# Kernel tuning notes

Measured on AMD Instinct MI355X. Metric: run time of the kernel, lower is better.

## Reference

```python
import jax, jax.numpy as jnp
import numpy as np

N, E, F_DIM = 30000, 480000, 256
CLS_HID, NUM_CLASS, GEN_HID, MI_HID, BATCH = 128, 16, 64, 128, 4096
COM_L1, COM_L2, LAM, ALPHA, TAU, EPS = 0.5, 0.5, 0.5, 1.0, 0.5, 1e-8


def _glorot(key, shape):
    scale = jnp.sqrt(2.0 / (shape[0] + shape[-1]))
    return scale * jax.random.normal(key, shape, dtype=jnp.float32)


def setup_inputs() -> dict:
    key = jax.random.key(0)
    ks = jax.random.split(key, 32)
    inp = {
        'feat': jax.random.normal(ks[0], (N, F_DIM), dtype=jnp.float32),
        'view1_indices': jax.random.randint(ks[1], (2, E), 0, N),
        'view1_values': jax.random.uniform(ks[2], (E,), dtype=jnp.float32),
        'view2_indices': jax.random.randint(ks[3], (2, E), 0, N),
        'view2_values': jax.random.uniform(ks[4], (E,), dtype=jnp.float32),
        'idx': jnp.sort(jax.random.randint(ks[5], (BATCH,), 0, N)),
        # GenView (v1 and v2): gen_gcn weight + gen_mlp (Linear(2*gen_hid, 1))
        'W_gen_v1': _glorot(ks[6], (F_DIM, GEN_HID)),
        'Wm_v1': _glorot(ks[7], (2 * GEN_HID, 1)),
        'bm_v1': jnp.zeros((1,), dtype=jnp.float32),
        'W_gen_v2': _glorot(ks[8], (F_DIM, GEN_HID)),
        'Wm_v2': _glorot(ks[9], (2 * GEN_HID, 1)),
        'bm_v2': jnp.zeros((1,), dtype=jnp.float32),
        # Classification: three two-layer GCN encoders (v1, v2, v)
        'W1_v1': _glorot(ks[10], (F_DIM, CLS_HID)), 'W2_v1': _glorot(ks[11], (CLS_HID, NUM_CLASS)),
        'W1_v2': _glorot(ks[12], (F_DIM, CLS_HID)), 'W2_v2': _glorot(ks[13], (CLS_HID, NUM_CLASS)),
        'W1_v': _glorot(ks[14], (F_DIM, CLS_HID)), 'W2_v': _glorot(ks[15], (CLS_HID, NUM_CLASS)),
        # MI_NCE: three single GCN layers + shared projection MLP
        'Wg': _glorot(ks[16], (F_DIM, MI_HID)),
        'Wg1': _glorot(ks[17], (F_DIM, MI_HID)),
        'Wg2': _glorot(ks[18], (F_DIM, MI_HID)),
        'Wp1': _glorot(ks[19], (MI_HID, MI_HID)), 'bp1': jnp.zeros((MI_HID,), dtype=jnp.float32),
        'Wp2': _glorot(ks[20], (MI_HID, MI_HID)), 'bp2': jnp.zeros((MI_HID,), dtype=jnp.float32),
    }
    return inp


def spmm(idx, vals, x, n):
    # sparse COO adj (idx [2,E], vals [E]) @ dense x [n,d]
    return jax.ops.segment_sum(vals[:, None] * x[idx[1]], idx[0], num_segments=n)


def gcn_layer(x, idx, vals, W, n, act):
    h = spmm(idx, vals, x @ W, n)
    return jax.nn.relu(h) if act else h


def two_layer(x, idx, vals, W1, W2, n):
    return gcn_layer(gcn_layer(x, idx, vals, W1, n, True), idx, vals, W2, n, False)


def sparse_row_softmax(scores, rows, n):
    m = jax.lax.stop_gradient(jax.ops.segment_max(scores, rows, num_segments=n))
    e = jnp.exp(scores - m[rows])
    s = jax.ops.segment_sum(e, rows, num_segments=n)
    return e / s[rows]


def gen_view(feat, idx, vals, Wg, Wm, bm, com_lambda, n):
    emb = gcn_layer(feat, idx, vals, Wg, n, True)
    ff = jnp.concatenate([emb[idx[0]], emb[idx[1]]], axis=-1)  # [E, 2*gen_hid]
    temp = (ff @ Wm + bm).reshape(-1)
    pi = sparse_row_softmax(temp, idx[0], n)  # torch.sparse.softmax(dim=1)
    return vals + com_lambda * pi  # same sparsity pattern as v_ori


def sym(idx, vals):
    # normalize1 (big=True): adj + adj.T as COO concat (duplicates sum in spmm)
    return jnp.concatenate([idx, idx[::-1]], axis=1), jnp.concatenate([vals, vals])


def get_weight(prob):
    top2 = jax.lax.top_k(prob, 2)[0]
    fir, sec = top2[:, 0], top2[:, 1]
    return jnp.exp(ALPHA * (LAM * jnp.log(fir + EPS) + (1.0 - LAM) * jnp.log(fir - sec + EPS)))


def contrast_cal(z1, z2):
    num = z1 @ z2.T
    den = jnp.linalg.norm(z1, axis=-1, keepdims=True) @ jnp.linalg.norm(z2, axis=-1, keepdims=True).T
    m12 = jnp.exp(num / den / TAU)
    m21 = m12.T
    l12 = -jnp.log(jnp.diag(m12 / (m12.sum(1, keepdims=True) + EPS)) + EPS).mean()
    l21 = -jnp.log(jnp.diag(m21 / (m21.sum(1, keepdims=True) + EPS)) + EPS).mean()
    return 0.5 * (l12 + l21)


def cogsl_forward(feat, view1_values, view2_values,
                  W_gen_v1, Wm_v1, bm_v1, W_gen_v2, Wm_v2, bm_v2,
                  W1_v1, W2_v1, W1_v2, W2_v2, W1_v, W2_v,
                  Wg, Wg1, Wg2, Wp1, bp1, Wp2, bp2,
                  view1_indices, view2_indices, idx):
    n = feat.shape[0]
    # View_Estimator (GenView + normalize1)
    nv1 = gen_view(feat, view1_indices, view1_values, W_gen_v1, Wm_v1, bm_v1, COM_L1, n)
    nv2 = gen_view(feat, view2_indices, view2_values, W_gen_v2, Wm_v2, bm_v2, COM_L2, n)
    i1, v1 = sym(view1_indices, nv1)
    i2, v2 = sym(view2_indices, nv2)
    # Classification on each generated view
    prob_v1 = jax.nn.softmax(two_layer(feat, i1, v1, W1_v1, W2_v1, n), axis=1)
    prob_v2 = jax.nn.softmax(two_layer(feat, i2, v2, W1_v2, W2_v2, n), axis=1)
    logits_v1 = jnp.log(prob_v1 + EPS)
    logits_v2 = jnp.log(prob_v2 + EPS)
    # Fusion: per-node convex combination of the two sparse views (row scaling)
    w1 = get_weight(prob_v1)
    w2 = get_weight(prob_v2)
    b1 = w1 / (w1 + w2)
    b2 = w2 / (w1 + w2)
    idx_f = jnp.concatenate([i1, i2], axis=1)
    vals_f = jnp.concatenate([b1[i1[0]] * v1, b2[i2[0]] * v2])
    prob_v = jax.nn.softmax(two_layer(feat, idx_f, vals_f, W1_v, W2_v, n), axis=1)
    logits_v = jnp.log(prob_v + EPS)
    # MI_NCE over [fused v, v1, v2], big=True -> sample `batch` nodes
    proj = lambda h: jax.nn.elu(h @ Wp1 + bp1) @ Wp2 + bp2
    ev = proj(gcn_layer(feat, idx_f, vals_f, Wg, n, True))[idx]
    e1 = proj(gcn_layer(feat, i1, v1, Wg1, n, True))[idx]
    e2 = proj(gcn_layer(feat, i2, v2, Wg2, n, True))[idx]
    vv1 = contrast_cal(ev, e1)
    vv2 = contrast_cal(ev, e2)
    v1v2 = contrast_cal(e1, e2)
    return jnp.concatenate([logits_v.ravel(), logits_v1.ravel(), logits_v2.ravel(),
                            jnp.stack([vv1, vv2, v1v2])])


def reference(feat, view1_indices, view1_values, view2_indices, view2_values, idx,
              W_gen_v1, Wm_v1, bm_v1, W_gen_v2, Wm_v2, bm_v2,
              W1_v1, W2_v1, W1_v2, W2_v2, W1_v, W2_v,
              Wg, Wg1, Wg2, Wp1, bp1, Wp2, bp2):
    return cogsl_forward(feat, view1_values, view2_values,
                         W_gen_v1, Wm_v1, bm_v1, W_gen_v2, Wm_v2, bm_v2,
                         W1_v1, W2_v1, W1_v2, W2_v2, W1_v, W2_v,
                         Wg, Wg1, Wg2, Wp1, bp1, Wp2, bp2,
                         view1_indices, view2_indices, idx)
```

## Files before the change

kernel.cpp:

```cpp
#include <hip/hip_runtime.h>
#include <math.h>

#define NN 30000
#define EE 480000
#define FD 256
#define CH 128
#define NCLS 16
#define GH 64
#define MH 128
#define BT 4096
#define EPSc 1e-8f
#define GBc ((NN + 127) / 128)
#define SPB8 ((NN + 7) / 8)
#define SPB16 ((NN + 15) / 16)
#define RBc ((BT + 15) / 16)

typedef __attribute__((ext_vector_type(8))) short short8;
typedef __attribute__((ext_vector_type(4))) float f32x4;

__device__ __forceinline__ unsigned short f2bf(float x) {
    unsigned b = __float_as_uint(x);
    unsigned r = b + 0x7FFFu + ((b >> 16) & 1u);
    return (unsigned short)(r >> 16);
}
__device__ __forceinline__ float bf2f(unsigned short h) {
    return __uint_as_float(((unsigned)h) << 16);
}
__device__ __forceinline__ float4 fma4(float s, float4 x, float4 a) {
    a.x = fmaf(s, x.x, a.x); a.y = fmaf(s, x.y, a.y);
    a.z = fmaf(s, x.z, a.z); a.w = fmaf(s, x.w, a.w);
    return a;
}

__global__ void split_bf16(const float* __restrict__ x, unsigned short* __restrict__ hi,
                           unsigned short* __restrict__ lo, long n) {
    long i = (long)blockIdx.x * 256 + threadIdx.x;
    if (i >= n) return;
    float v = x[i];
    unsigned short h = f2bf(v);
    hi[i] = h;
    lo[i] = f2bf(v - bf2f(h));
}

struct WSArgs {
    const float* s[8];
    unsigned short* h[8];
    unsigned short* l[8];
};
__global__ void wsplit_all(WSArgs a) {
    constexpr int NNp[8] = {64, 64, 128, 128, 128, 128, 128, 128};
    constexpr int OFF[9] = {0, 16384, 32768, 65536, 98304, 131072, 163840, 196608, 229376};
    int i = blockIdx.x * 256 + threadIdx.x;
    if (i >= 229376) return;
    int w = 0;
#pragma unroll
    for (int t = 1; t < 8; t++) if (i >= OFF[t]) w = t;
    int j = i - OFF[w];
    int N = NNp[w];
    int k = j / N, n = j % N;
    float v = a.s[w][j];
    unsigned short hh = f2bf(v);
    a.h[w][(size_t)n * 256 + k] = hh;
    a.l[w][(size_t)n * 256 + k] = f2bf(v - bf2f(hh));
}

template <int NT, bool OUT16>
__device__ __forceinline__ void gemm3_body(
    unsigned short* sm, int bx,
    const unsigned short* __restrict__ Ahi, const unsigned short* __restrict__ Alo,
    const unsigned short* __restrict__ BThi, const unsigned short* __restrict__ BTlo,
    int K, void* __restrict__ Cv, int Cstride, int M)
{
    unsigned short* Ah = sm;
    unsigned short* Al = Ah + 128 * 40;
    unsigned short* Bh = Al + 128 * 40;
    unsigned short* Bl = Bh + NT * 16 * 40;
    int t = threadIdx.x;
    int w = t >> 6, l = t & 63;
    int lane = l & 15, quad = l >> 4;
    int row0 = bx * 128;
    f32x4 acc[2][NT];
#pragma unroll
    for (int s = 0; s < 2; s++)
#pragma unroll
        for (int n = 0; n < NT; n++) acc[s][n] = (f32x4)(0.f);

    int ar = t >> 1, ako = (t & 1) << 4;
    int nkc = K >> 5;
    for (int kc = 0; kc < nkc; kc++) {
        int kb = kc << 5;
        {
            int gr = row0 + ar;
            float4 h0, h1, l0, l1;
            if (gr < M) {
                const float4* pH = (const float4*)&Ahi[(size_t)gr * K + kb + ako];
                const float4* pL = (const float4*)&Alo[(size_t)gr * K + kb + ako];
                h0 = pH[0]; h1 = pH[1]; l0 = pL[0]; l1 = pL[1];
            } else {
                h0 = h1 = l0 = l1 = make_float4(0.f, 0.f, 0.f, 0.f);
            }
            float4* dH = (float4*)&Ah[ar * 40 + ako];
            dH[0] = h0; dH[1] = h1;
            float4* dL = (float4*)&Al[ar * 40 + ako];
            dL[0] = l0; dL[1] = l1;
        }
        if (ar < NT * 16) {
            const float4* pH = (const float4*)&BThi[(size_t)ar * K + kb + ako];
            const float4* pL = (const float4*)&BTlo[(size_t)ar * K + kb + ako];
            float4 h0 = pH[0], h1 = pH[1], l0 = pL[0], l1 = pL[1];
            float4* dH = (float4*)&Bh[ar * 40 + ako];
            dH[0] = h0; dH[1] = h1;
            float4* dL = (float4*)&Bl[ar * 40 + ako];
            dL[0] = l0; dL[1] = l1;
        }
        __syncthreads();
        short8 aH[2], aL[2];
#pragma unroll
        for (int s = 0; s < 2; s++) {
            int r = w * 32 + s * 16 + lane;
            aH[s] = *(const short8*)&Ah[r * 40 + quad * 8];
            aL[s] = *(const short8*)&Al[r * 40 + quad * 8];
        }
#pragma unroll
        for (int n = 0; n < NT; n++) {
            int r = n * 16 + lane;
            short8 bH = *(const short8*)&Bh[r * 40 + quad * 8];
            short8 bL = *(const short8*)&Bl[r * 40 + quad * 8];
#pragma unroll
            for (int s = 0; s < 2; s++) {
                acc[s][n] = __builtin_amdgcn_mfma_f32_16x16x32_bf16(aH[s], bH, acc[s][n], 0, 0, 0);
                acc[s][n] = __builtin_amdgcn_mfma_f32_16x16x32_bf16(aH[s], bL, acc[s][n], 0, 0, 0);
                acc[s][n] = __builtin_amdgcn_mfma_f32_16x16x32_bf16(aL[s], bH, acc[s][n], 0, 0, 0);
            }
        }
        __syncthreads();
    }
#pragma unroll
    for (int s = 0; s < 2; s++) {
        int rb = row0 + w * 32 + s * 16 + quad * 4;
#pragma unroll
        for (int reg = 0; reg < 4; reg++) {
            int gr = rb + reg;
            if (gr >= M) continue;
#pragma unroll
            for (int n = 0; n < NT; n++) {
                if (OUT16)
                    ((unsigned short*)Cv)[(size_t)gr * Cstride + n * 16 + lane] = f2bf(acc[s][n][reg]);
                else
                    ((float*)Cv)[(size_t)gr * Cstride + n * 16 + lane] = acc[s][n][reg];
            }
        }
    }
}

template <int NT, bool OUT16>
__device__ __forceinline__ void gemm1_body(
    unsigned short* sm, int bx,
    const unsigned short* __restrict__ Ahi,
    const unsigned short* __restrict__ BThi,
    int K, void* __restrict__ Cv, int Cstride, int M)
{
    unsigned short* Ah = sm;
    unsigned short* Bh = Ah + 128 * 40;
    int t = threadIdx.x;
    int w = t >> 6, l = t & 63;
    int lane = l & 15, quad = l >> 4;
    int row0 = bx * 128;
    f32x4 acc[2][NT];
#pragma unroll
    for (int s = 0; s < 2; s++)
#pragma unroll
        for (int n = 0; n < NT; n++) acc[s][n] = (f32x4)(0.f);

    int ar = t >> 1, ako = (t & 1) << 4;
    int nkc = K >> 5;
    for (int kc = 0; kc < nkc; kc++) {
        int kb = kc << 5;
        {
            int gr = row0 + ar;
            float4 h0, h1;
            if (gr < M) {
                const float4* pH = (const float4*)&Ahi[(size_t)gr * K + kb + ako];
                h0 = pH[0]; h1 = pH[1];
            } else {
                h0 = h1 = make_float4(0.f, 0.f, 0.f, 0.f);
            }
            float4* dH = (float4*)&Ah[ar * 40 + ako];
            dH[0] = h0; dH[1] = h1;
        }
        if (ar < NT * 16) {
            const float4* pH = (const float4*)&BThi[(size_t)ar * K + kb + ako];
            float4 h0 = pH[0], h1 = pH[1];
            float4* dH = (float4*)&Bh[ar * 40 + ako];
            dH[0] = h0; dH[1] = h1;
        }
        __syncthreads();
        short8 aH[2];
#pragma unroll
        for (int s = 0; s < 2; s++)
            aH[s] = *(const short8*)&Ah[(w * 32 + s * 16 + lane) * 40 + quad * 8];
#pragma unroll
        for (int n = 0; n < NT; n++) {
            short8 bH = *(const short8*)&Bh[(n * 16 + lane) * 40 + quad * 8];
#pragma unroll
            for (int s = 0; s < 2; s++)
                acc[s][n] = __builtin_amdgcn_mfma_f32_16x16x32_bf16(aH[s], bH, acc[s][n], 0, 0, 0);
        }
        __syncthreads();
    }
#pragma unroll
    for (int s = 0; s < 2; s++) {
        int rb = row0 + w * 32 + s * 16 + quad * 4;
#pragma unroll
        for (int reg = 0; reg < 4; reg++) {
            int gr = rb + reg;
            if (gr >= M) continue;
#pragma unroll
            for (int n = 0; n < NT; n++) {
                if (OUT16)
                    ((unsigned short*)Cv)[(size_t)gr * Cstride + n * 16 + lane] = f2bf(acc[s][n][reg]);
                else
                    ((float*)Cv)[(size_t)gr * Cstride + n * 16 + lane] = acc[s][n][reg];
            }
        }
    }
}

__global__ __launch_bounds__(256) void mega0(
    const int* __restrict__ i1, const int* __restrict__ i2, int* __restrict__ cnt,
    int* __restrict__ sd1, int* __restrict__ sd2,
    int* __restrict__ sc1, int* __restrict__ sc2,
    const unsigned short* __restrict__ feat_hi,
    const unsigned short* __restrict__ w1vh, unsigned short* __restrict__ Ph2,
    const unsigned short* __restrict__ wgallh, unsigned short* __restrict__ Pmi16)
{
    __shared__ unsigned short sm[128 * 40 + 8 * 16 * 40];
    int b = blockIdx.x;
    if (b < GBc) {
        gemm1_body<8, true>(sm, b, feat_hi, w1vh, FD, Ph2, 128, NN);
        return;
    }
    b -= GBc;
    if (b < 3 * GBc) {
        int y = b / GBc, bx = b % GBc;
        gemm1_body<8, true>(sm, bx, feat_hi, wgallh + (size_t)y * 32768,
                            FD, Pmi16 + (size_t)y * 128, 384, NN);
        return;
    }
    b -= 3 * GBc;
    int e = b * 256 + threadIdx.x;
    if (e >= EE) return;
    int r1 = i1[e], c1 = i1[EE + e];
    int r2 = i2[e], c2 = i2[EE + e];
    sd1[e] = atomicAdd(&cnt[r1], 1);
    sd2[e] = atomicAdd(&cnt[NN + r2], 1);
    sc1[e] = atomicAdd(&cnt[2 * NN + c1], 1);
    sc2[e] = atomicAdd(&cnt[3 * NN + c2], 1);
}

__global__ __launch_bounds__(256) void mega1(
    const int* __restrict__ i1, const float* __restrict__ v1,
    const int* __restrict__ i2, const float* __restrict__ v2,
    const int* __restrict__ sd1, const int* __restrict__ sd2,
    const int* __restrict__ sc1, const int* __restrict__ sc2,
    const int* __restrict__ rp4,
    int2* __restrict__ ed1, int2* __restrict__ ec1,
    int2* __restrict__ ed2, int2* __restrict__ ec2,
    const unsigned short* __restrict__ feat_hi, const unsigned short* __restrict__ feat_lo,
    const unsigned short* __restrict__ wgen12h, const unsigned short* __restrict__ wgen12l,
    float* __restrict__ Pg,
    const unsigned short* __restrict__ w1pairh, const unsigned short* __restrict__ w1pairl,
    float* __restrict__ P01)
{
    __shared__ unsigned short sm[128 * 40 * 2 + 8 * 16 * 40 * 2];
    int b = blockIdx.x;
    if (b < GBc) {
        gemm3_body<8, false>(sm, b, feat_hi, feat_lo, wgen12h, wgen12l, FD, Pg, 128, NN);
        return;
    }
    b -= GBc;
    if (b < 2 * GBc) {
        int y = b / GBc, bx = b % GBc;
        gemm3_body<8, false>(sm, bx, feat_hi, feat_lo,
                             w1pairh + (size_t)y * 32768, w1pairl + (size_t)y * 32768,
                             FD, P01 + (size_t)y * 128, 256, NN);
        return;
    }
    b -= 2 * GBc;
    int e = b * 256 + threadIdx.x;
    if (e >= EE) return;
    const int* rp_d1 = rp4;
    const int* rp_d2 = rp4 + (NN + 1);
    const int* rp_c1 = rp4 + 2 * (NN + 1);
    const int* rp_c2 = rp4 + 3 * (NN + 1);
    int r = i1[e], c = i1[EE + e];
    int p = rp_d1[r] + sd1[e];
    ed1[p] = make_int2(c, __float_as_int(v1[e]));
    ec1[rp_c1[c] + sc1[e]] = make_int2(r, p);
    r = i2[e]; c = i2[EE + e];
    p = rp_d2[r] + sd2[e];
    ed2[p] = make_int2(c, __float_as_int(v2[e]));
    ec2[rp_c2[c] + sc2[e]] = make_int2(r, p);
}

__global__ __launch_bounds__(256) void contrast_direct(
    const unsigned short* __restrict__ z16, float* __restrict__ stats)
{
    int p = blockIdx.z;
    int pa = (p == 2) ? 1 : 0;
    int pb = (p == 0) ? 1 : 2;
    const unsigned short* A = z16 + (size_t)pa * BT * MH;
    const unsigned short* B = z16 + (size_t)pb * BT * MH;
    float* diag = stats + (size_t)p * 3 * BT;
    float* rs = diag + BT;
    float* cs = rs + BT;
    int t = threadIdx.x;
    int w = t >> 6, l = t & 63, m = l & 15, quad = l >> 4;
    int i0 = blockIdx.y * 128, j0 = blockIdx.x * 128;
// ... 127 lines not shown
template <int STR4>
__device__ __forceinline__ void gath_dir_f32(
    const int* __restrict__ rp, const int2* __restrict__ ed, int row,
    const float4* __restrict__ x4, int xo, float4* a)
{
    int p0 = rp[row], p1 = rp[row + 1];
    int j = p0;
    for (; j + 8 <= p1; j += 8) {
        int2 q0 = ed[j], q1 = ed[j+1], q2 = ed[j+2], q3 = ed[j+3];
        int2 q4 = ed[j+4], q5 = ed[j+5], q6 = ed[j+6], q7 = ed[j+7];
        float4 x0 = x4[(size_t)q0.x * STR4 + xo];
        float4 x1 = x4[(size_t)q1.x * STR4 + xo];
        float4 x2 = x4[(size_t)q2.x * STR4 + xo];
        float4 x3 = x4[(size_t)q3.x * STR4 + xo];
        float4 x5 = x4[(size_t)q4.x * STR4 + xo];
        float4 x6 = x4[(size_t)q5.x * STR4 + xo];
        float4 x7 = x4[(size_t)q6.x * STR4 + xo];
        float4 x8 = x4[(size_t)q7.x * STR4 + xo];
        a[0] = fma4(__int_as_float(q0.y), x0, a[0]);
        a[1] = fma4(__int_as_float(q1.y), x1, a[1]);
        a[2] = fma4(__int_as_float(q2.y), x2, a[2]);
        a[3] = fma4(__int_as_float(q3.y), x3, a[3]);
        a[0] = fma4(__int_as_float(q4.y), x5, a[0]);
        a[1] = fma4(__int_as_float(q5.y), x6, a[1]);
        a[2] = fma4(__int_as_float(q6.y), x7, a[2]);
        a[3] = fma4(__int_as_float(q7.y), x8, a[3]);
    }
    for (; j + 4 <= p1; j += 4) {
        int2 q0 = ed[j], q1 = ed[j+1], q2 = ed[j+2], q3 = ed[j+3];
        a[0] = fma4(__int_as_float(q0.y), x4[(size_t)q0.x * STR4 + xo], a[0]);
        a[1] = fma4(__int_as_float(q1.y), x4[(size_t)q1.x * STR4 + xo], a[1]);
        a[2] = fma4(__int_as_float(q2.y), x4[(size_t)q2.x * STR4 + xo], a[2]);
        a[3] = fma4(__int_as_float(q3.y), x4[(size_t)q3.x * STR4 + xo], a[3]);
    }
    for (; j < p1; j++) {
        int2 q = ed[j];
        a[0] = fma4(__int_as_float(q.y), x4[(size_t)q.x * STR4 + xo], a[0]);
    }
}
template <int STR4>
__device__ __forceinline__ void gath_csc_f32(
    const int* __restrict__ rp, const int2* __restrict__ ec, const float* __restrict__ nvd,
    int row, const float4* __restrict__ x4, int xo, float4* a)
{
    int p0 = rp[row], p1 = rp[row + 1];
    int j = p0;
    for (; j + 8 <= p1; j += 8) {
        int2 q0 = ec[j], q1 = ec[j+1], q2 = ec[j+2], q3 = ec[j+3];
        int2 q4 = ec[j+4], q5 = ec[j+5], q6 = ec[j+6], q7 = ec[j+7];
        float4 x0 = x4[(size_t)q0.x * STR4 + xo];
        float4 x1 = x4[(size_t)q1.x * STR4 + xo];
        float4 x2 = x4[(size_t)q2.x * STR4 + xo];
        float4 x3 = x4[(size_t)q3.x * STR4 + xo];
        float4 x5 = x4[(size_t)q4.x * STR4 + xo];
        float4 x6 = x4[(size_t)q5.x * STR4 + xo];
        float4 x7 = x4[(size_t)q6.x * STR4 + xo];
        float4 x8 = x4[(size_t)q7.x * STR4 + xo];
        float v0 = nvd[q0.y], v1 = nvd[q1.y], v2 = nvd[q2.y], v3 = nvd[q3.y];
        float v4 = nvd[q4.y], v5 = nvd[q5.y], v6 = nvd[q6.y], v7 = nvd[q7.y];
        a[0] = fma4(v0, x0, a[0]);
        a[1] = fma4(v1, x1, a[1]);
        a[2] = fma4(v2, x2, a[2]);
        a[3] = fma4(v3, x3, a[3]);
        a[0] = fma4(v4, x5, a[0]);
        a[1] = fma4(v5, x6, a[1]);
        a[2] = fma4(v6, x7, a[2]);
        a[3] = fma4(v7, x8, a[3]);
    }
    for (; j + 4 <= p1; j += 4) {
        int2 q0 = ec[j], q1 = ec[j+1], q2 = ec[j+2], q3 = ec[j+3];
        float v0 = nvd[q0.y], v1 = nvd[q1.y], v2 = nvd[q2.y], v3 = nvd[q3.y];
        a[0] = fma4(v0, x4[(size_t)q0.x * STR4 + xo], a[0]);
        a[1] = fma4(v1, x4[(size_t)q1.x * STR4 + xo], a[1]);
        a[2] = fma4(v2, x4[(size_t)q2.x * STR4 + xo], a[2]);
        a[3] = fma4(v3, x4[(size_t)q3.x * STR4 + xo], a[3]);
    }
    for (; j < p1; j++) {
        int2 q = ec[j];
        a[0] = fma4(nvd[q.y], x4[(size_t)q.x * STR4 + xo], a[0]);
    }
}

__global__ __launch_bounds__(256) void spmm64_scores(
    const int* __restrict__ rp_d, const int2* __restrict__ e1, const int2* __restrict__ e2,
    const float* __restrict__ Pg, const float* __restrict__ Wm1,
    const float* __restrict__ Wm2, float* __restrict__ sb)
{
    int y = blockIdx.y;
    const int* rp = rp_d + y * (NN + 1);
    const int2* arr = y ? e2 : e1;
    int row = blockIdx.x * 16 + threadIdx.x / 16;
    int o = threadIdx.x % 16;
    if (row >= NN) return;
    float4 a[4] = {};
    gath_dir_f32<32>(rp, arr, row, (const float4*)Pg, y * 16 + o, a);
    float4 r;
    r.x = fmaxf((a[0].x + a[1].x) + (a[2].x + a[3].x), 0.f);
    r.y = fmaxf((a[0].y + a[1].y) + (a[2].y + a[3].y), 0.f);
    r.z = fmaxf((a[0].z + a[1].z) + (a[2].z + a[3].z), 0.f);
    r.w = fmaxf((a[0].w + a[1].w) + (a[2].w + a[3].w), 0.f);
    const float* Wmh = (y ? Wm2 : Wm1) + GH;
    float part = r.x * Wmh[o * 4] + r.y * Wmh[o * 4 + 1]
               + r.z * Wmh[o * 4 + 2] + r.w * Wmh[o * 4 + 3];
    part += __shfl_xor(part, 1); part += __shfl_xor(part, 2);
    part += __shfl_xor(part, 4); part += __shfl_xor(part, 8);
    if (o == 0) sb[y * NN + row] = part;
}

__device__ __forceinline__ void softmax16_epi(
    float4 r, int node, float* __restrict__ logits, float* __restrict__ wout)
{
    int o = threadIdx.x & 3;
    float mx = fmaxf(fmaxf(r.x, r.y), fmaxf(r.z, r.w));
    mx = fmaxf(mx, __shfl_xor(mx, 1));
    mx = fmaxf(mx, __shfl_xor(mx, 2));
    float e0 = expf(r.x - mx), e1 = expf(r.y - mx), e2 = expf(r.z - mx), e3 = expf(r.w - mx);
    float s = (e0 + e1) + (e2 + e3);
    s += __shfl_xor(s, 1);
    s += __shfl_xor(s, 2);
    float inv = 1.f / s;
    float p0 = e0 * inv, p1 = e1 * inv, p2 = e2 * inv, p3 = e3 * inv;
    float4 lg;
    lg.x = logf(p0 + EPSc); lg.y = logf(p1 + EPSc);
    lg.z = logf(p2 + EPSc); lg.w = logf(p3 + EPSc);
    ((float4*)logits)[(size_t)node * 4 + o] = lg;
    if (wout) {
        float f = p0, se = -1.f;
        if (p1 > f) { se = f; f = p1; } else se = p1;
        if (p2 > f) { se = f; f = p2; } else if (p2 > se) se = p2;
        if (p3 > f) { se = f; f = p3; } else if (p3 > se) se = p3;
#pragma unroll
        for (int d = 1; d <= 2; d <<= 1) {
            float of = __shfl_xor(f, d), os = __shfl_xor(se, d);
            if (of > f) { se = fmaxf(f, os); f = of; }
            else se = fmaxf(se, of);
        }
        if (o == 0)
            wout[node] = expf(0.5f * logf(f + EPSc) + 0.5f * logf(f - se + EPSc));
    }
}

__global__ __launch_bounds__(256) void spmm16_softmax_pair(
    const int* __restrict__ rp_d, const int* __restrict__ rp_c,
    const int2* __restrict__ ed1, const int2* __restrict__ ec1, const float* __restrict__ nvd1,
    const int2* __restrict__ ed2, const int2* __restrict__ ec2, const float* __restrict__ nvd2,
    const float* __restrict__ R01, float* __restrict__ logits_base, float* __restrict__ w12)
{
    int y = blockIdx.y;
    const int* rpd = rp_d + y * (NN + 1);
    const int* rpc = rp_c + y * (NN + 1);
    const int2* ed = y ? ed2 : ed1;
    const int2* ec = y ? ec2 : ec1;
    const float* nvd = y ? nvd2 : nvd1;
    int row = blockIdx.x * 64 + threadIdx.x / 4;
    int o = threadIdx.x % 4;
    if (row >= NN) return;
    const float4* x4 = (const float4*)(R01 + (size_t)y * NN * 16);
    float4 a[4] = {};
    gath_dir_f32<4>(rpd, ed, row, x4, o, a);
    gath_csc_f32<4>(rpc, ec, nvd, row, x4, o, a);
    float4 r;
    r.x = (a[0].x + a[1].x) + (a[2].x + a[3].x);
    r.y = (a[0].y + a[1].y) + (a[2].y + a[3].y);
    r.z = (a[0].z + a[1].z) + (a[2].z + a[3].z);
    r.w = (a[0].w + a[1].w) + (a[2].w + a[3].w);
    softmax16_epi(r, row, logits_base + (size_t)y * NN * NCLS, w12 + (size_t)y * NN);
}

__global__ __launch_bounds__(256) void spmm16_fused_softmax(
    const int* __restrict__ rp_d, const int* __restrict__ rp_c,
    const int2* __restrict__ ed1, const int2* __restrict__ ec1, const float* __restrict__ nvd1,
    const int2* __restrict__ ed2, const int2* __restrict__ ec2, const float* __restrict__ nvd2,
    const float* __restrict__ w12, const float* __restrict__ x, float* __restrict__ logits)
{
    int row = blockIdx.x * 64 + threadIdx.x / 4;
    int o = threadIdx.x % 4;
    if (row >= NN) return;
    const float4* x4 = (const float4*)x;
    float4 a[4] = {};
    gath_dir_f32<4>(rp_d, ed1, row, x4, o, a);
    gath_csc_f32<4>(rp_c, ec1, nvd1, row, x4, o, a);
    float4 s1;
    s1.x = (a[0].x + a[1].x) + (a[2].x + a[3].x);
    s1.y = (a[0].y + a[1].y) + (a[2].y + a[3].y);
    s1.z = (a[0].z + a[1].z) + (a[2].z + a[3].z);
    s1.w = (a[0].w + a[1].w) + (a[2].w + a[3].w);
    float4 b[4] = {};
    gath_dir_f32<4>(rp_d + (NN + 1), ed2, row, x4, o, b);
    gath_csc_f32<4>(rp_c + (NN + 1), ec2, nvd2, row, x4, o, b);
    float4 s2;
    s2.x = (b[0].x + b[1].x) + (b[2].x + b[3].x);
    s2.y = (b[0].y + b[1].y) + (b[2].y + b[3].y);
    s2.z = (b[0].z + b[1].z) + (b[2].z + b[3].z);
    s2.w = (b[0].w + b[1].w) + (b[2].w + b[3].w);
    float wa = w12[row], wb = w12[NN + row];
    float inv = 1.f / (wa + wb);
    float w1 = wa * inv, w2 = wb * inv;
    float4 r;
    r.x = w1 * s1.x + w2 * s2.x;
    r.y = w1 * s1.y + w2 * s2.y;
    r.z = w1 * s1.z + w2 * s2.z;
    r.w = w1 * s1.w + w2 * s2.w;
    softmax16_epi(r, row, logits, nullptr);
}

__device__ __forceinline__ void gath_dir_b16(
    const int* __restrict__ rp, const int2* __restrict__ ed, int row,
    const unsigned short* __restrict__ X, int xstride, int o, float* acc)
{
    int p0 = rp[row], p1 = rp[row + 1];
    int j = p0;
    for (; j + 8 <= p1; j += 8) {
        int2 q[8]; short8 x[8];
#pragma unroll
        for (int e = 0; e < 8; e++) q[e] = ed[j + e];
#pragma unroll
        for (int e = 0; e < 8; e++)
            x[e] = *(const short8*)&X[(size_t)q[e].x * xstride + o * 8];
#pragma unroll
        for (int e = 0; e < 8; e++) {
            float v = __int_as_float(q[e].y);
#pragma unroll
            for (int k = 0; k < 8; k++)
                acc[k] = fmaf(v, bf2f((unsigned short)x[e][k]), acc[k]);
        }
    }
    for (; j + 4 <= p1; j += 4) {
        int2 q0 = ed[j], q1 = ed[j+1], q2 = ed[j+2], q3 = ed[j+3];
        short8 x0 = *(const short8*)&X[(size_t)q0.x * xstride + o * 8];
        short8 x1 = *(const short8*)&X[(size_t)q1.x * xstride + o * 8];
        short8 x2 = *(const short8*)&X[(size_t)q2.x * xstride + o * 8];
        short8 x3 = *(const short8*)&X[(size_t)q3.x * xstride + o * 8];
        float v0 = __int_as_float(q0.y), v1 = __int_as_float(q1.y);
        float v2 = __int_as_float(q2.y), v3 = __int_as_float(q3.y);
#pragma unroll
        for (int k = 0; k < 8; k++) {
            acc[k] = fmaf(v0, bf2f((unsigned short)x0[k]), acc[k]);
            acc[k] = fmaf(v1, bf2f((unsigned short)x1[k]), acc[k]);
            acc[k] = fmaf(v2, bf2f((unsigned short)x2[k]), acc[k]);
            acc[k] = fmaf(v3, bf2f((unsigned short)x3[k]), acc[k]);
        }
    }
    for (; j < p1; j++) {
        int2 q = ed[j];
        short8 xv = *(const short8*)&X[(size_t)q.x * xstride + o * 8];
        float v = __int_as_float(q.y);
#pragma unroll
        for (int k = 0; k < 8; k++)
            acc[k] = fmaf(v, bf2f((unsigned short)xv[k]), acc[k]);
    }
}
__device__ __forceinline__ void gath_csc_b16(
    const int* __restrict__ rp, const int2* __restrict__ ec, const float* __restrict__ nvd,
    int row, const unsigned short* __restrict__ X, int xstride, int o, float* acc)
{
    int p0 = rp[row], p1 = rp[row + 1];
    int j = p0;
    for (; j + 8 <= p1; j += 8) {
        int2 q[8]; short8 x[8];
#pragma unroll
        for (int e = 0; e < 8; e++) q[e] = ec[j + e];
#pragma unroll
        for (int e = 0; e < 8; e++)
            x[e] = *(const short8*)&X[(size_t)q[e].x * xstride + o * 8];
        float v[8];
#pragma unroll
        for (int e = 0; e < 8; e++) v[e] = nvd[q[e].y];
#pragma unroll
        for (int e = 0; e < 8; e++) {
#pragma unroll
            for (int k = 0; k < 8; k++)
                acc[k] = fmaf(v[e], bf2f((unsigned short)x[e][k]), acc[k]);
        }
    }
    for (; j + 4 <= p1; j += 4) {
        int2 q0 = ec[j], q1 = ec[j+1], q2 = ec[j+2], q3 = ec[j+3];
        short8 x0 = *(const short8*)&X[(size_t)q0.x * xstride + o * 8];
        short8 x1 = *(const short8*)&X[(size_t)q1.x * xstride + o * 8];
        short8 x2 = *(const short8*)&X[(size_t)q2.x * xstride + o * 8];
        short8 x3 = *(const short8*)&X[(size_t)q3.x * xstride + o * 8];
        float v0 = nvd[q0.y], v1 = nvd[q1.y], v2 = nvd[q2.y], v3 = nvd[q3.y];
#pragma unroll
        for (int k = 0; k < 8; k++) {
            acc[k] = fmaf(v0, bf2f((unsigned short)x0[k]), acc[k]);
            acc[k] = fmaf(v1, bf2f((unsigned short)x1[k]), acc[k]);
            acc[k] = fmaf(v2, bf2f((unsigned short)x2[k]), acc[k]);
            acc[k] = fmaf(v3, bf2f((unsigned short)x3[k]), acc[k]);
        }
    }
    for (; j < p1; j++) {
        int2 q = ec[j];
        short8 xv = *(const short8*)&X[(size_t)q.x * xstride + o * 8];
        float v = nvd[q.y];
#pragma unroll
        for (int k = 0; k < 8; k++)
            acc[k] = fmaf(v, bf2f((unsigned short)xv[k]), acc[k]);
    }
}

__device__ __forceinline__ void rows_b16_body(
    int bx, int y, const int* __restrict__ rp_d, const int* __restrict__ rp_c,
    const int2* __restrict__ ed1, const int2* __restrict__ ec1, const float* __restrict__ nvd1,
    const int2* __restrict__ ed2, const int2* __restrict__ ec2, const float* __restrict__ nvd2,
    const float* __restrict__ w12, const int* __restrict__ rows,
    const unsigned short* __restrict__ Pmi, float* __restrict__ zQ)
{
    int ri = bx * 16 + threadIdx.x / 16;
    int o = threadIdx.x % 16;
    if (ri >= BT) return;
    int node = rows[ri];
    int xoff = (y == 0) ? 0 : ((y == 1) ? 128 : 256);
    const unsigned short* X = Pmi + xoff;
    float acc[8] = {};
    if (y == 0) {
        float a1[8] = {}, a2[8] = {};
        gath_dir_b16(rp_d, ed1, node, X, 384, o, a1);
        gath_csc_b16(rp_c, ec1, nvd1, node, X, 384, o, a1);
        gath_dir_b16(rp_d + (NN + 1), ed2, node, X, 384, o, a2);
        gath_csc_b16(rp_c + (NN + 1), ec2, nvd2, node, X, 384, o, a2);
        float wa = w12[node], wb = w12[NN + node];
        float inv = 1.f / (wa + wb);
        float w1 = wa * inv, w2 = wb * inv;
#pragma unroll
        for (int k = 0; k < 8; k++) acc[k] = w1 * a1[k] + w2 * a2[k];
    } else if (y == 1) {
        gath_dir_b16(rp_d, ed1, node, X, 384, o, acc);
        gath_csc_b16(rp_c, ec1, nvd1, node, X, 384, o, acc);
    } else {
        gath_dir_b16(rp_d + (NN + 1), ed2, node, X, 384, o, acc);
        gath_csc_b16(rp_c + (NN + 1), ec2, nvd2, node, X, 384, o, acc);
    }
    float* out = zQ + ((size_t)y * BT + ri) * 128 + o * 8;
#pragma unroll
    for (int k = 0; k < 8; k++) out[k] = fmaxf(acc[k], 0.f);
}

__device__ __forceinline__ void spmm128f_body(
    float* sm, int bx, int y, const int* __restrict__ rp_d, const int* __restrict__ rp_c,
    const int2* __restrict__ ed, const int2* __restrict__ ec, const float* __restrict__ nvd,
    const float* __restrict__ P01, const float* __restrict__ W2, float* __restrict__ R01)
{
    float* W2s = sm;
    float* Qs  = sm + 2048;
    for (int i = threadIdx.x; i < 2048; i += 256) W2s[i] = W2[i];
    int r = threadIdx.x / 32;
    int o = threadIdx.x % 32;
    int row = bx * 8 + r;
    float4 a[4] = {};
    if (row < NN) {
        gath_dir_f32<64>(rp_d + y * (NN + 1), ed, row, (const float4*)P01, y * 32 + o, a);
        gath_csc_f32<64>(rp_c + y * (NN + 1), ec, nvd, row, (const float4*)P01, y * 32 + o, a);
    }
    float4 q;
    q.x = fmaxf((a[0].x + a[1].x) + (a[2].x + a[3].x), 0.f);
    q.y = fmaxf((a[0].y + a[1].y) + (a[2].y + a[3].y), 0.f);
    q.z = fmaxf((a[0].z + a[1].z) + (a[2].z + a[3].z), 0.f);
    q.w = fmaxf((a[0].w + a[1].w) + (a[2].w + a[3].w), 0.f);
    *(float4*)&Qs[r * 128 + o * 4] = q;
    __syncthreads();
    int t = threadIdx.x;
    if (t < 128) {
        int rr = t >> 4, c = t & 15;
        int grow = bx * 8 + rr;
        if (grow < NN) {
            float acc = 0.f;
            const float* qrow = &Qs[rr * 128];
#pragma unroll 8
            for (int k = 0; k < 128; k++)
                acc = fmaf(qrow[k], W2s[k * 16 + c], acc);
            R01[((size_t)y * NN + grow) * 16 + c] = acc;
        }
    }
}

__device__ __forceinline__ void fused128b2_body(
    float* sm, int bx, const int* __restrict__ rp_d, const int* __restrict__ rp_c,
    const int2* __restrict__ ed1, const int2* __restrict__ ec1, const float* __restrict__ nvd1,
    const int2* __restrict__ ed2, const int2* __restrict__ ec2, const float* __restrict__ nvd2,
    const float* __restrict__ w12, const unsigned short* __restrict__ Ph2,
    const float* __restrict__ W2v, float* __restrict__ R2)
{
    float* W2s = sm;
    float* Qs  = sm + 2048;
    for (int i = threadIdx.x; i < 2048; i += 256) W2s[i] = W2v[i];
    int r = threadIdx.x / 16;
    int o = threadIdx.x % 16;
    int row = bx * 16 + r;
    float a1[8] = {}, a2[8] = {};
    float w1 = 0.f, w2 = 0.f;
    if (row < NN) {
        gath_dir_b16(rp_d, ed1, row, Ph2, 128, o, a1);
        gath_csc_b16(rp_c, ec1, nvd1, row, Ph2, 128, o, a1);
        gath_dir_b16(rp_d + (NN + 1), ed2, row, Ph2, 128, o, a2);
        gath_csc_b16(rp_c + (NN + 1), ec2, nvd2, row, Ph2, 128, o, a2);
        float wa = w12[row], wb = w12[NN + row];
        float inv = 1.f / (wa + wb);
        w1 = wa * inv; w2 = wb * inv;
    }
#pragma unroll
    for (int k = 0; k < 8; k++)
        Qs[r * 128 + o * 8 + k] = fmaxf(w1 * a1[k] + w2 * a2[k], 0.f);
    __syncthreads();
    int t = threadIdx.x;
    int rr = t >> 4, c = t & 15;
    int grow = bx * 16 + rr;
    if (grow < NN) {
        float acc = 0.f;
        const float* qrow = &Qs[rr * 128];
#pragma unroll 8
        for (int k = 0; k < 128; k++)
            acc = fmaf(qrow[k], W2s[k * 16 + c], acc);
        R2[(size_t)grow * 16 + c] = acc;
    }
}

__global__ __launch_bounds__(256) void mega2(
    const int* __restrict__ rp_d, const int* __restrict__ rp_c,
    const int2* __restrict__ ed1, const int2* __restrict__ ec1, const float* __restrict__ nvd1,
    const int2* __restrict__ ed2, const int2* __restrict__ ec2, const float* __restrict__ nvd2,
    const float* __restrict__ P01, const float* __restrict__ W2v1, const float* __restrict__ W2v2,
    float* __restrict__ R01,
    const int* __restrict__ rows, const unsigned short* __restrict__ Pmi,
    float* __restrict__ zQ)
{
    __shared__ float sm[2048 + 8 * 128];
    int b = blockIdx.x;
    if (b < 2 * SPB8) {
        int y = b / SPB8;
        spmm128f_body(sm, b % SPB8, y, rp_d, rp_c, y ? ed2 : ed1, y ? ec2 : ec1,
                      y ? nvd2 : nvd1, P01, y ? W2v2 : W2v1, R01);
        return;
    }
    b -= 2 * SPB8;
    int y = 1 + b / RBc;
    rows_b16_body(b % RBc, y, rp_d, rp_c, ed1, ec1, nvd1, ed2, ec2, nvd2,
                  nullptr, rows, Pmi, zQ);
}

__global__ __launch_bounds__(256) void mega3(
    const int* __restrict__ rp_d, const int* __restrict__ rp_c,
    const int2* __restrict__ ed1, const int2* __restrict__ ec1, const float* __restrict__ nvd1,
    const int2* __restrict__ ed2, const int2* __restrict__ ec2, const float* __restrict__ nvd2,
    const float* __restrict__ w12, const unsigned short* __restrict__ Ph2,
    const float* __restrict__ W2v, float* __restrict__ R2,
    const int* __restrict__ rows, const unsigned short* __restrict__ Pmi,
    float* __restrict__ zQ)
{
    __shared__ float sm[2048 + 16 * 128];
    int b = blockIdx.x;
    if (b < SPB16) {
        fused128b2_body(sm, b, rp_d, rp_c, ed1, ec1, nvd1, ed2, ec2, nvd2,
                        w12, Ph2, W2v, R2);
        return;
    }
    rows_b16_body(b - SPB16, 0, rp_d, rp_c, ed1, ec1, nvd1, ed2, ec2, nvd2,
                  w12, rows, Pmi, zQ);
}

__global__ __launch_bounds__(256) void proj_norm8(
    const float* __restrict__ zQ,
    const float* __restrict__ Wp1, const float* __restrict__ bp1,
    const float* __restrict__ Wp2, const float* __restrict__ bp2,
    unsigned short* __restrict__ z16)
{
    __shared__ float g[8 * MH], u[8 * MH];
    __shared__ float red[4][4];
    int t = threadIdx.x;
    size_t base = (size_t)blockIdx.y * BT + (size_t)blockIdx.x * 8;
    for (int idx = t; idx < 8 * MH; idx += 256)
        g[idx] = zQ[(base + (idx >> 7)) * MH + (idx & 127)];
    __syncthreads();
    int col = t & 127;
    int rh = t >> 7;
    float acc[4];
    float b1 = bp1[col];
#pragma unroll
    for (int rr = 0; rr < 4; rr++) acc[rr] = b1;
    for (int k = 0; k < MH; k++) {
        float wk = Wp1[k * MH + col];
#pragma unroll
        for (int rr = 0; rr < 4; rr++)
            acc[rr] = fmaf(g[(rh * 4 + rr) * MH + k], wk, acc[rr]);
    }
#pragma unroll
    for (int rr = 0; rr < 4; rr++)
        u[(rh * 4 + rr) * MH + col] = acc[rr] > 0.f ? acc[rr] : (expf(acc[rr]) - 1.f);
    __syncthreads();
    float z[4];
    float b2 = bp2[col];
#pragma unroll
    for (int rr = 0; rr < 4; rr++) z[rr] = b2;
    for (int k = 0; k < MH; k++) {
        float wk = Wp2[k * MH + col];
#pragma unroll
        for (int rr = 0; rr < 4; rr++)
            z[rr] = fmaf(u[(rh * 4 + rr) * MH + k], wk, z[rr]);
    }
    float sq[4];
#pragma unroll
    for (int rr = 0; rr < 4; rr++) sq[rr] = z[rr] * z[rr];
#pragma unroll
    for (int off = 32; off; off >>= 1) {
#pragma unroll
        for (int rr = 0; rr < 4; rr++) sq[rr] += __shfl_xor(sq[rr], off);
    }
    int w = t >> 6;
    if ((t & 63) == 0) {
#pragma unroll
        for (int rr = 0; rr < 4; rr++) red[w][rr] = sq[rr];
    }
    __syncthreads();
#pragma unroll
    for (int rr = 0; rr < 4; rr++) {
        float nrm = sqrtf(red[rh * 2][rr] + red[rh * 2 + 1][rr]);
        z16[(base + rh * 4 + rr) * MH + col] = f2bf(z[rr] / nrm);
    }
}

__global__ void contrast_reduce(const float* __restrict__ stats, float* __restrict__ out3)
{
    int p = blockIdx.x, t = threadIdx.x;
    const float* diag = stats + (size_t)p * 3 * BT;
    const float* rs = diag + BT;
    const float* cs = rs + BT;
    float s1 = 0.f, s2 = 0.f;
    for (int i = t; i < BT; i += 256) {
        float d = diag[i];
        s1 += logf(d / (rs[i] + EPSc) + EPSc);
        s2 += logf(d / (cs[i] + EPSc) + EPSc);
    }
#pragma unroll
    for (int off = 32; off; off >>= 1) { s1 += __shfl_down(s1, off); s2 += __shfl_down(s2, off); }
    __shared__ float sh[8];
    if ((t & 63) == 0) { sh[(t >> 6) * 2] = s1; sh[(t >> 6) * 2 + 1] = s2; }
    __syncthreads();
    if (t == 0) {
        float a = sh[0] + sh[2] + sh[4] + sh[6];
        float b = sh[1] + sh[3] + sh[5] + sh[7];
        out3[p] = 0.5f * (-a / BT - b / BT);
    }
}

extern "C" void kernel_launch(void* const* d_in, const int* in_sizes, int n_in,
                              void* d_out, int out_size, void* d_ws, size_t ws_size,
                              hipStream_t stream)
{
    const float* feat   = (const float*)d_in[0];
    const int*   ind1   = (const int*)d_in[1];
    const float* vals1  = (const float*)d_in[2];
    const int*   ind2   = (const int*)d_in[3];
    const float* vals2  = (const float*)d_in[4];
    const int*   idxb   = (const int*)d_in[5];
    const float* Wm1    = (const float*)d_in[7];
    const float* Wm2    = (const float*)d_in[10];
    const float* W2_v1  = (const float*)d_in[13];
    const float* W2_v2  = (const float*)d_in[15];
    const float* W2_v   = (const float*)d_in[17];
    const float* Wp1    = (const float*)d_in[21];
    const float* bp1    = (const float*)d_in[22];
    const float* Wp2    = (const float*)d_in[23];
    const float* bp2    = (const float*)d_in[24];
    float* dout = (float*)d_out;

    float* ws = (float*)d_ws;
    size_t off = 0;
    auto alloc = [&](size_t n) { n = (n + 3) & ~(size_t)3; float* p = ws + off; off += n; return p; };
    auto alloc_s = [&](size_t n) { return (unsigned short*)alloc((n + 1) / 2); };

    float* pool = alloc(16000000);
    float* Pg   = pool;
    float* P01  = pool + 3840000;
    float* R01  = pool + 11520000;
    float* zQ   = pool + 12480000;
    float* R2   = pool;

    unsigned short* feat_hi = alloc_s((size_t)NN * FD);
    unsigned short* feat_lo = alloc_s((size_t)NN * FD);
    unsigned short* Ph2d    = alloc_s((size_t)NN * CH);
    unsigned short* Pmi16d  = alloc_s((size_t)NN * 384);
    float* sb   = alloc(2 * NN);
    float* w12  = alloc(2 * NN);
    float* stats = alloc((size_t)3 * 3 * BT);
    unsigned short* z16 = alloc_s((size_t)3 * BT * MH);
    int2* ed1 = (int2*)alloc(2 * (size_t)EE);
    int2* ed2 = (int2*)alloc(2 * (size_t)EE);
    int2* ec1 = (int2*)alloc(2 * (size_t)EE);
    int2* ec2 = (int2*)alloc(2 * (size_t)EE);
    float* nvd1 = alloc(EE);
    float* nvd2 = alloc(EE);
    int* sd1 = (int*)alloc(EE);
    int* sd2 = (int*)alloc(EE);
    int* sc1 = (int*)alloc(EE);
    int* sc2 = (int*)alloc(EE);
    int* rp4  = (int*)alloc(4 * (NN + 1));
    int* cnt4 = (int*)alloc(4 * NN);
    int* bsum = (int*)alloc(128);
    int* rp_d = rp4;
    int* rp_c = rp4 + 2 * (NN + 1);
    unsigned short* wgen12h = alloc_s(32768); unsigned short* wgen12l = alloc_s(32768);
    unsigned short* w1pairh = alloc_s(65536); unsigned short* w1pairl = alloc_s(65536);
    unsigned short* w1vh    = alloc_s(32768); unsigned short* w1vl    = alloc_s(32768);
    unsigned short* wgallh  = alloc_s(98304); unsigned short* wgalll  = alloc_s(98304);

    const int NB = (NN + 1 + 1023) / 1024;
    const int NCNT = (EE + 255) / 256;

    hipMemsetAsync(cnt4, 0, 4 * NN * 4, stream);
    split_bf16<<<((long)NN * FD + 255) / 256, 256, 0, stream>>>(feat, feat_hi, feat_lo, (long)NN * FD);
    {
        WSArgs a;
        a.s[0] = (const float*)d_in[6];  a.h[0] = wgen12h;          a.l[0] = wgen12l;
        a.s[1] = (const float*)d_in[9];  a.h[1] = wgen12h + 16384;  a.l[1] = wgen12l + 16384;
        a.s[2] = (const float*)d_in[12]; a.h[2] = w1pairh;          a.l[2] = w1pairl;
        a.s[3] = (const float*)d_in[14]; a.h[3] = w1pairh + 32768;  a.l[3] = w1pairl + 32768;
        a.s[4] = (const float*)d_in[16]; a.h[4] = w1vh;             a.l[4] = w1vl;
        a.s[5] = (const float*)d_in[18]; a.h[5] = wgallh;           a.l[5] = wgalll;
        a.s[6] = (const float*)d_in[19]; a.h[6] = wgallh + 32768;   a.l[6] = wgalll + 32768;
        a.s[7] = (const float*)d_in[20]; a.h[7] = wgallh + 65536;   a.l[7] = wgalll + 65536;
        wsplit_all<<<(229376 + 255) / 256, 256, 0, stream>>>(a);
    }

    mega0<<<4 * GBc + NCNT, 256, 0, stream>>>(ind1, ind2, cnt4, sd1, sd2, sc1, sc2,
                                              feat_hi, w1vh, Ph2d, wgallh, Pmi16d);

    scan_block4<<<dim3(NB, 4), 1024, 0, stream>>>(cnt4, rp4, bsum);
    scan_bsum4<<<4, 64, 0, stream>>>(bsum, NB);
    scan_add4<<<dim3(NB, 4), 1024, 0, stream>>>(bsum, rp4);

    mega1<<<3 * GBc + NCNT, 256, 0, stream>>>(ind1, vals1, ind2, vals2,
                                              sd1, sd2, sc1, sc2, rp4,
                                              ed1, ec1, ed2, ec2,
                                              feat_hi, feat_lo, wgen12h, wgen12l, Pg,
                                              w1pairh, w1pairl, P01);

    spmm64_scores<<<dim3((NN + 15) / 16, 2), 256, 0, stream>>>(rp_d, ed1, ed2, Pg, Wm1, Wm2, sb);
    gen_nv<<<dim3((NN + 255) / 256, 2), 256, 0, stream>>>(rp_d, ed1, ed2, sb, nvd1, nvd2);

    mega2<<<2 * SPB8 + 2 * RBc, 256, 0, stream>>>(rp_d, rp_c, ed1, ec1, nvd1,
                                                  ed2, ec2, nvd2, P01, W2_v1, W2_v2,
                                                  R01, idxb, Pmi16d, zQ);

    spmm16_softmax_pair<<<dim3((NN + 63) / 64, 2), 256, 0, stream>>>(
        rp_d, rp_c, ed1, ec1, nvd1, ed2, ec2, nvd2, R01, dout + (size_t)NN * NCLS, w12);

    mega3<<<SPB16 + RBc, 256, 0, stream>>>(rp_d, rp_c, ed1, ec1, nvd1, ed2, ec2, nvd2,
                                           w12, Ph2d, W2_v, R2, idxb, Pmi16d, zQ);

    spmm16_fused_softmax<<<(NN + 63) / 64, 256, 0, stream>>>(
        rp_d, rp_c, ed1, ec1, nvd1, ed2, ec2, nvd2, w12, R2, dout);

    proj_norm8<<<dim3(BT / 8, 3), 256, 0, stream>>>(zQ, Wp1, bp1, Wp2, bp2, z16);
    hipMemsetAsync(stats, 0, (size_t)3 * 3 * BT * 4, stream);
    contrast_direct<<<dim3(32, 32, 3), 256, 0, stream>>>(z16, stats);
    contrast_reduce<<<3, 256, 0, stream>>>(stats, dout + (size_t)3 * NN * NCLS);
}
```

Baseline: 774.6 us.

## Hoist w12-independent fused-view gathers into earlier mega kernel, combine later

After: 883.3 us. 14.0% more time.

```diff
diff --git a/kernel.cpp b/kernel.cpp
--- a/kernel.cpp
+++ b/kernel.cpp
@@ -14,6 +14,7 @@
 #define SPB8 ((NN + 7) / 8)
 #define SPB16 ((NN + 15) / 16)
 #define RBc ((BT + 15) / 16)
+#define NOX (SPB16 + 3 * RBc)
 
 typedef __attribute__((ext_vector_type(8))) short short8;
 typedef __attribute__((ext_vector_type(4))) float f32x4;
@@ -747,28 +748,17 @@
     int bx, int y, const int* __restrict__ rp_d, const int* __restrict__ rp_c,
     const int2* __restrict__ ed1, const int2* __restrict__ ec1, const float* __restrict__ nvd1,
     const int2* __restrict__ ed2, const int2* __restrict__ ec2, const float* __restrict__ nvd2,
-    const float* __restrict__ w12, const int* __restrict__ rows,
+    const int* __restrict__ rows,
     const unsigned short* __restrict__ Pmi, float* __restrict__ zQ)
 {
     int ri = bx * 16 + threadIdx.x / 16;
     int o = threadIdx.x % 16;
     if (ri >= BT) return;
     int node = rows[ri];
-    int xoff = (y == 0) ? 0 : ((y == 1) ? 128 : 256);
+    int xoff = (y == 1) ? 128 : 256;
     const unsigned short* X = Pmi + xoff;
     float acc[8] = {};
-    if (y == 0) {
-        float a1[8] = {}, a2[8] = {};
-        gath_dir_b16(rp_d, ed1, node, X, 384, o, a1);
-        gath_csc_b16(rp_c, ec1, nvd1, node, X, 384, o, a1);
-        gath_dir_b16(rp_d + (NN + 1), ed2, node, X, 384, o, a2);
-        gath_csc_b16(rp_c + (NN + 1), ec2, nvd2, node, X, 384, o, a2);
-        float wa = w12[node], wb = w12[NN + node];
-        float inv = 1.f / (wa + wb);
-        float w1 = wa * inv, w2 = wb * inv;
-#pragma unroll
-        for (int k = 0; k < 8; k++) acc[k] = w1 * a1[k] + w2 * a2[k];
-    } else if (y == 1) {
+    if (y == 1) {
         gath_dir_b16(rp_d, ed1, node, X, 384, o, acc);
         gath_csc_b16(rp_c, ec1, nvd1, node, X, 384, o, acc);
     } else {
@@ -778,6 +768,54 @@
     float* out = zQ + ((size_t)y * BT + ri) * 128 + o * 8;
 #pragma unroll
     for (int k = 0; k < 8; k++) out[k] = fmaxf(acc[k], 0.f);
+}
+
+__device__ __forceinline__ void rows0_gather_body(
+    int bx, const int* __restrict__ rp_d, const int* __restrict__ rp_c,
+    const int2* __restrict__ ed1, const int2* __restrict__ ec1, const float* __restrict__ nvd1,
+    const int2* __restrict__ ed2, const int2* __restrict__ ec2, const float* __restrict__ nvd2,
+    const int* __restrict__ rows, const unsigned short* __restrict__ Pmi,
+    float* __restrict__ G1, float* __restrict__ G2)
+{
+    int ri = bx * 16 + threadIdx.x / 16;
+    int o = threadIdx.x % 16;
+    if (ri >= BT) return;
+    int node = rows[ri];
+    float g1[8] = {}, g2[8] = {};
+    gath_dir_b16(rp_d, ed1, node, Pmi, 384, o, g1);
+    gath_csc_b16(rp_c, ec1, nvd1, node, Pmi, 384, o, g1);
+    gath_dir_b16(rp_d + (NN + 1), ed2, node, Pmi, 384, o, g2);
+    gath_csc_b16(rp_c + (NN + 1), ec2, nvd2, node, Pmi, 384, o, g2);
+    float* o1 = G1 + (size_t)ri * 128 + o * 8;
+    float* o2 = G2 + (size_t)ri * 128 + o * 8;
+    *(float4*)&o1[0] = make_float4(g1[0], g1[1], g1[2], g1[3]);
+    *(float4*)&o1[4] = make_float4(g1[4], g1[5], g1[6], g1[7]);
+    *(float4*)&o2[0] = make_float4(g2[0], g2[1], g2[2], g2[3]);
+    *(float4*)&o2[4] = make_float4(g2[4], g2[5], g2[6], g2[7]);
+}
+
+__device__ __forceinline__ void b2gather_body(
+    int bx, const int* __restrict__ rp_d, const int* __restrict__ rp_c,
+    const int2* __restrict__ ed1, const int2* __restrict__ ec1, const float* __restrict__ nvd1,
+    const int2* __restrict__ ed2, const int2* __restrict__ ec2, const float* __restrict__ nvd2,
+    const unsigned short* __restrict__ Ph2,
+    float* __restrict__ A1, float* __restrict__ A2)
+{
+    int r = threadIdx.x / 16;
+    int o = threadIdx.x % 16;
+    int row = bx * 16 + r;
+    if (row >= NN) return;
+    float a1[8] = {}, a2[8] = {};
+    gath_dir_b16(rp_d, ed1, row, Ph2, 128, o, a1);
+    gath_csc_b16(rp_c, ec1, nvd1, row, Ph2, 128, o, a1);
+    gath_dir_b16(rp_d + (NN + 1), ed2, row, Ph2, 128, o, a2);
+    gath_csc_b16(rp_c + (NN + 1), ec2, nvd2, row, Ph2, 128, o, a2);
+    float* o1 = A1 + (size_t)row * 128 + o * 8;
+    float* o2 = A2 + (size_t)row * 128 + o * 8;
+    *(float4*)&o1[0] = make_float4(a1[0], a1[1], a1[2], a1[3]);
+    *(float4*)&o1[4] = make_float4(a1[4], a1[5], a1[6], a1[7]);
+    *(float4*)&o2[0] = make_float4(a2[0], a2[1], a2[2], a2[3]);
+    *(float4*)&o2[4] = make_float4(a2[4], a2[5], a2[6], a2[7]);
 }
 
 __device__ __forceinline__ void spmm128f_body(
@@ -818,88 +856,95 @@
     }
 }
 
-__device__ __forceinline__ void fused128b2_body(
-    float* sm, int bx, const int* __restrict__ rp_d, const int* __restrict__ rp_c,
+__global__ __launch_bounds__(256) void mega23(
+    const int* __restrict__ rp_d, const int* __restrict__ rp_c,
     const int2* __restrict__ ed1, const int2* __restrict__ ec1, const float* __restrict__ nvd1,
     const int2* __restrict__ ed2, const int2* __restrict__ ec2, const float* __restrict__ nvd2,
-    const float* __restrict__ w12, const unsigned short* __restrict__ Ph2,
-    const float* __restrict__ W2v, float* __restrict__ R2)
-{
-    float* W2s = sm;
-    float* Qs  = sm + 2048;
-    for (int i = threadIdx.x; i < 2048; i += 256) W2s[i] = W2v[i];
+    const float* __restrict__ P01, const float* __restrict__ W2v1, const float* __restrict__ W2v2,
+    float* __restrict__ R01,
+    const int* __restrict__ rows, const unsigned short* __restrict__ Pmi,
+    float* __restrict__ zQ,
+    const unsigned short* __restrict__ Ph2,
+    float* __restrict__ A1, float* __restrict__ A2,
+    float* __restrict__ G1, float* __restrict__ G2)
+{
+    __shared__ float sm[2048 + 8 * 128];
+    int b = blockIdx.x;
+    int u = b >> 2, r = b & 3;
+    if (r == 3) {
+        if (u < SPB16) {
+            b2gather_body(u, rp_d, rp_c, ed1, ec1, nvd1, ed2, ec2, nvd2, Ph2, A1, A2);
+            return;
+        }
+        u -= SPB16;
+        if (u < 2 * RBc) {
+            int y = 1 + u / RBc;
+            rows_b16_body(u % RBc, y, rp_d, rp_c, ed1, ec1, nvd1, ed2, ec2, nvd2,
+                          rows, Pmi, zQ);
+            return;
+        }
+        u -= 2 * RBc;
+        rows0_gather_body(u, rp_d, rp_c, ed1, ec1, nvd1, ed2, ec2, nvd2,
+                          rows, Pmi, G1, G2);
+        return;
+    }
+    int s = u * 3 + r;
+    if (s >= 2 * SPB8) return;
+    int y = s / SPB8;
+    spmm128f_body(sm, s % SPB8, y, rp_d, rp_c, y ? ed2 : ed1, y ? ec2 : ec1,
+                  y ? nvd2 : nvd1, P01, y ? W2v2 : W2v1, R01);
+}
+
+__global__ __launch_bounds__(256) void combineB2(
+    const float* __restrict__ w12,
+    const float* __restrict__ A1, const float* __restrict__ A2,
+    const float* __restrict__ W2v, float* __restrict__ R2,
+    const int* __restrict__ rows,
+    const float* __restrict__ G1, const float* __restrict__ G2,
+    float* __restrict__ zQ)
+{
+    __shared__ float sm[2048 + 16 * 128];
+    int b = blockIdx.x;
     int r = threadIdx.x / 16;
     int o = threadIdx.x % 16;
-    int row = bx * 16 + r;
-    float a1[8] = {}, a2[8] = {};
-    float w1 = 0.f, w2 = 0.f;
-    if (row < NN) {
-        gath_dir_b16(rp_d, ed1, row, Ph2, 128, o, a1);
-        gath_csc_b16(rp_c, ec1, nvd1, row, Ph2, 128, o, a1);
-        gath_dir_b16(rp_d + (NN + 1), ed2, row, Ph2, 128, o, a2);
-        gath_csc_b16(rp_c + (NN + 1), ec2, nvd2, row, Ph2, 128, o, a2);
+    if (b < SPB16) {
+        float* W2s = sm;
+        float* Qs  = sm + 2048;
+        for (int i = threadIdx.x; i < 2048; i += 256) W2s[i] = W2v[i];
+        int row = b * 16 + r;
         float wa = w12[row], wb = w12[NN + row];
         float inv = 1.f / (wa + wb);
-        w1 = wa * inv; w2 = wb * inv;
-    }
-#pragma unroll
-    for (int k = 0; k < 8; k++)
-        Qs[r * 128 + o * 8 + k] = fmaxf(w1 * a1[k] + w2 * a2[k], 0.f);
-    __syncthreads();
-    int t = threadIdx.x;
-    int rr = t >> 4, c = t & 15;
-    int grow = bx * 16 + rr;
-    if (grow < NN) {
+        float w1 = wa * inv, w2 = wb * inv;
+        const float* p1 = A1 + (size_t)row * 128 + o * 8;
+        const float* p2 = A2 + (size_t)row * 128 + o * 8;
+#pragma unroll
+        for (int k = 0; k < 8; k++)
+            Qs[r * 128 + o * 8 + k] = fmaxf(w1 * p1[k] + w2 * p2[k], 0.f);
+        __syncthreads();
+        int t = threadIdx.x;
+        int rr = t >> 4, c = t & 15;
+        int grow = b * 16 + rr;
         float acc = 0.f;
         const float* qrow = &Qs[rr * 128];
 #pragma unroll 8
         for (int k = 0; k < 128; k++)
             acc = fmaf(qrow[k], W2s[k * 16 + c], acc);
         R2[(size_t)grow * 16 + c] = acc;
-    }
-}
-
-__global__ __launch_bounds__(256) void mega2(
-    const int* __restrict__ rp_d, const int* __restrict__ rp_c,
-    const int2* __restrict__ ed1, const int2* __restrict__ ec1, const float* __restrict__ nvd1,
-    const int2* __restrict__ ed2, const int2* __restrict__ ec2, const float* __restrict__ nvd2,
-    const float* __restrict__ P01, const float* __restrict__ W2v1, const float* __restrict__ W2v2,
-    float* __restrict__ R01,
-    const int* __restrict__ rows, const unsigned short* __restrict__ Pmi,
-    float* __restrict__ zQ)
-{
-    __shared__ float sm[2048 + 8 * 128];
-    int b = blockIdx.x;
-    if (b < 2 * SPB8) {
-        int y = b / SPB8;
-        spmm128f_body(sm, b % SPB8, y, rp_d, rp_c, y ? ed2 : ed1, y ? ec2 : ec1,
-                      y ? nvd2 : nvd1, P01, y ? W2v2 : W2v1, R01);
         return;
     }
-    b -= 2 * SPB8;
-    int y = 1 + b / RBc;
-    rows_b16_body(b % RBc, y, rp_d, rp_c, ed1, ec1, nvd1, ed2, ec2, nvd2,
-                  nullptr, rows, Pmi, zQ);
-}
-
-__global__ __launch_bounds__(256) void mega3(
-    const int* __restrict__ rp_d, const int* __restrict__ rp_c,
-    const int2* __restrict__ ed1, const int2* __restrict__ ec1, const float* __restrict__ nvd1,
-    const int2* __restrict__ ed2, const int2* __restrict__ ec2, const float* __restrict__ nvd2,
-    const float* __restrict__ w12, const unsigned short* __restrict__ Ph2,
-    const float* __restrict__ W2v, float* __restrict__ R2,
-    const int* __restrict__ rows, const unsigned short* __restrict__ Pmi,
-    float* __restrict__ zQ)
-{
-    __shared__ float sm[2048 + 16 * 128];
-    int b = blockIdx.x;
-    if (b < SPB16) {
-        fused128b2_body(sm, b, rp_d, rp_c, ed1, ec1, nvd1, ed2, ec2, nvd2,
-                        w12, Ph2, W2v, R2);
-        return;
-    }
-    rows_b16_body(b - SPB16, 0, rp_d, rp_c, ed1, ec1, nvd1, ed2, ec2, nvd2,
-                  w12, rows, Pmi, zQ);
+    b -= SPB16;
+    int ri = b * 16 + r;
+    if (ri >= BT) return;
+    int node = rows[ri];
+    float wa = w12[node], wb = w12[NN + node];
+    float inv = 1.f / (wa + wb);
+    float w1 = wa * inv, w2 = wb * inv;
+    const float* p1 = G1 + (size_t)ri * 128 + o * 8;
+    const float* p2 = G2 + (size_t)ri * 128 + o * 8;
+    float* out = zQ + (size_t)ri * 128 + o * 8;
+#pragma unroll
+    for (int k = 0; k < 8; k++)
+        out[k] = fmaxf(w1 * p1[k] + w2 * p2[k], 0.f);
 }
 
 __global__ __launch_bounds__(256) void proj_norm8(
@@ -1017,10 +1062,14 @@
     float* P01  = pool + 3840000;
     float* R01  = pool + 11520000;
     float* zQ   = pool + 12480000;
-    float* R2   = pool;
+    float* A1   = pool;
+    float* G1   = pool + 14052864;
+    float* G2   = pool + 14577152;
+    float* R2   = pool + 15101440;
 
     unsigned short* feat_hi = alloc_s((size_t)NN * FD);
     unsigned short* feat_lo = alloc_s((size_t)NN * FD);
+    float* A2 = (float*)feat_hi;
     unsigned short* Ph2d    = alloc_s((size_t)NN * CH);
     unsigned short* Pmi16d  = alloc_s((size_t)NN * 384);
     float* sb   = alloc(2 * NN);
@@ -1081,15 +1130,15 @@
     spmm64_scores<<<dim3((NN + 15) / 16, 2), 256, 0, stream>>>(rp_d, ed1, ed2, Pg, Wm1, Wm2, sb);
     gen_nv<<<dim3((NN + 255) / 256, 2), 256, 0, stream>>>(rp_d, ed1, ed2, sb, nvd1, nvd2);
 
-    mega2<<<2 * SPB8 + 2 * RBc, 256, 0, stream>>>(rp_d, rp_c, ed1, ec1, nvd1,
-                                                  ed2, ec2, nvd2, P01, W2_v1, W2_v2,
-                                                  R01, idxb, Pmi16d, zQ);
+    mega23<<<4 * NOX, 256, 0, stream>>>(rp_d, rp_c, ed1, ec1, nvd1,
+                                        ed2, ec2, nvd2, P01, W2_v1, W2_v2,
+                                        R01, idxb, Pmi16d, zQ,
+                                        Ph2d, A1, A2, G1, G2);
 
     spmm16_softmax_pair<<<dim3((NN + 63) / 64, 2), 256, 0, stream>>>(
         rp_d, rp_c, ed1, ec1, nvd1, ed2, ec2, nvd2, R01, dout + (size_t)NN * NCLS, w12);
 
-    mega3<<<SPB16 + RBc, 256, 0, stream>>>(rp_d, rp_c, ed1, ec1, nvd1, ed2, ec2, nvd2,
-                                           w12, Ph2d, W2_v, R2, idxb, Pmi16d, zQ);
+    combineB2<<<SPB16 + RBc, 256, 0, stream>>>(w12, A1, A2, W2_v, R2, idxb, G1, G2, zQ);
 
     spmm16_fused_softmax<<<(NN + 63) / 64, 256, 0, stream>>>(
         rp_d, rp_c, ed1, ec1, nvd1, ed2, ec2, nvd2, w12, R2, dout);
```
